# Kernel optimization log

Measured on AMD Instinct MI355X. Metric: run time of the kernel, lower is better.

Reference implementation:

```python
import jax, jax.numpy as jnp
import numpy as np

H = 64; V = 64; INNER = 24; SEQ = 32; CAP = 8
LR = 0.05; BETA1 = 0.9; BETA2 = 0.999; EPS = 1e-8
B = 16384


def setup_inputs():
    key = jax.random.key(0)
    ks = jax.random.split(key, 16)
    def w(k, shape, fan_in):
        return (jax.random.uniform(k, shape, jnp.float32, -1., 1.) / np.sqrt(fan_in)).astype(jnp.float32)
    return {
        "seqs": jax.random.randint(ks[0], (B, SEQ), 0, V),
        "embed": jax.random.normal(ks[1], (V, H), jnp.float32),
        "ff_w1": w(ks[2], (H, 2 * H), H),
        "ff_b1": w(ks[3], (2 * H,), H),
        "ff_w2": w(ks[4], (2 * H, H), 2 * H),
        "ff_b2": w(ks[5], (H,), 2 * H),
        "ln_g": jnp.ones((H,), jnp.float32),
        "ln_b": jnp.zeros((H,), jnp.float32),
        "scorer_w": w(ks[6], (2 * H, 1), 2 * H),
        "scorer_b": w(ks[7], (1,), 2 * H),
        "mlp_w1": w(ks[8], (H, INNER), H),
        "mlp_b1": w(ks[9], (INNER,), H),
        "mlp_w2": w(ks[10], (INNER, H), INNER),
        "mlp_b2": w(ks[11], (H,), INNER),
        "out_w": w(ks[12], (H, V), H),
        "out_b": w(ks[13], (V,), H),
    }


def reference(seqs, embed, ff_w1, ff_b1, ff_w2, ff_b2, ln_g, ln_b,
              scorer_w, scorer_b, mlp_w1, mlp_b1, mlp_w2, mlp_b2, out_w, out_b):
    sg = jax.lax.stop_gradient
    tmap = jax.tree_util.tree_map

    def encode(tok):  # [S] int -> [S,H]
        e = embed[tok]
        f = jnp.maximum(e @ ff_w1 + ff_b1, 0.) @ ff_w2 + ff_b2
        x = e + f
        mu = jnp.mean(x, -1, keepdims=True)
        var = jnp.mean((x - mu) ** 2, -1, keepdims=True)
        return (x - mu) * jax.lax.rsqrt(var + 1e-5) * ln_g + ln_b

    def mlp_fwd(p, x):
        w1, b1, w2, b2 = p
        return jnp.maximum(x @ w1 + b1, 0.) @ w2 + b2

    # tmp MLP is initialized from a detached copy of base mlp params
    base = (sg(mlp_w1), sg(mlp_b1), sg(mlp_w2), sg(mlp_b2))
    ar = jnp.arange(CAP - 1)

    def per_sample(tok):
        h = encode(tok)  # [32,64]
        # pairs: key at even t (0..28), value at odd t (1..29) -> 15 pairs, detached
        keys = sg(h[0:SEQ - 2:2])
        vals = sg(h[1:SEQ - 1:2])
        scores = sg(jnp.concatenate([keys, vals], -1) @ scorer_w[:, 0] + scorer_b[0])  # [15]
        # buffer fills with first CAP pairs, then evict-min (first occurrence) + append
        def evict(carry, new):
            bk, bv, bs = carry
            nk, nv, ns = new
            mi = jnp.argmin(bs)  # first min index, like python min()
            idx = jnp.where(ar < mi, ar, ar + 1)  # pop(mi) shift-left
            return (jnp.concatenate([bk[idx], nk[None]], 0),
                    jnp.concatenate([bv[idx], nv[None]], 0),
                    jnp.concatenate([bs[idx], ns[None]], 0)), None
        (bk, bv, _), _ = jax.lax.scan(
            evict, (keys[:CAP], vals[:CAP], scores[:CAP]),
            (keys[CAP:], vals[CAP:], scores[CAP:]))
        # inner-loop Adam finetune over the CAP buffered (k,v) pairs, in order
        loss = lambda p, k, v: jnp.mean((mlp_fwd(p, k) - v) ** 2)
        def adam(carry, kv):
            p, m, v, t = carry
            g = jax.grad(loss)(p, kv[0], kv[1])
            t = t + 1.
            m = tmap(lambda a, b: BETA1 * a + (1. - BETA1) * b, m, g)
            v = tmap(lambda a, b: BETA2 * a + (1. - BETA2) * b * b, v, g)
            p = tmap(lambda pp, mm, vv: pp - LR * (mm / (1. - BETA1 ** t)) /
                     (jnp.sqrt(vv / (1. - BETA2 ** t)) + EPS), p, m, v)
            return (p, m, v, t), None
        z = tmap(jnp.zeros_like, base)
        (p, _, _, _), _ = jax.lax.scan(adam, (base, z, z, jnp.float32(0.)), (bk, bv))
        # query = encoding of token SEQ-2, through finetuned MLP then output head
        return mlp_fwd(p, h[SEQ - 2]) @ out_w + out_b  # [V]

    return jax.vmap(per_sample)(seqs)  # [B, V]
```

## Files before the change

### kernel.cpp

```cpp
#include <hip/hip_runtime.h>

#define LRC   0.05f
#define B1C   0.9f
#define B2C   0.999f

typedef float v2f __attribute__((ext_vector_type(2)));

__device__ __forceinline__ v2f splat(float s) { v2f r; r.x = s; r.y = s; return r; }

__device__ __forceinline__ float rlane(float v, int l) {
  return __int_as_float(__builtin_amdgcn_readlane(__float_as_int(v), l));
}

template <int CTRL, int RMASK, bool BC>
__device__ __forceinline__ float dpp_add(float x) {
  int y = __builtin_amdgcn_update_dpp(0, __float_as_int(x), CTRL, RMASK, 0xF, BC);
  return x + __int_as_float(y);
}

__device__ __forceinline__ float xrow_sum1(float x) {
#if __has_builtin(__builtin_amdgcn_permlane16_swap)
  {
    unsigned xi = __float_as_uint(x);
    auto a = __builtin_amdgcn_permlane16_swap(xi, xi, false, false);
    x = __uint_as_float(a[0]) + __uint_as_float(a[1]);
  }
#else
  x = x + __int_as_float(__builtin_amdgcn_ds_swizzle(__float_as_int(x), 0x401F));
#endif
#if __has_builtin(__builtin_amdgcn_permlane32_swap)
  {
    unsigned xi = __float_as_uint(x);
    auto b = __builtin_amdgcn_permlane32_swap(xi, xi, false, false);
    x = __uint_as_float(b[0]) + __uint_as_float(b[1]);
  }
#else
  {
    int a32 = ((((int)threadIdx.x & 63) << 2) + 128) & 255;
    x = x + __int_as_float(__builtin_amdgcn_ds_bpermute(a32, __float_as_int(x)));
  }
#endif
  return x;
}

template <int N>
__device__ __forceinline__ void row_sum_batch(float* a) {
  #pragma unroll
  for (int c = 0; c < N; ++c) a[c] = dpp_add<0x121, 0xF, true>(a[c]);
  #pragma unroll
  for (int c = 0; c < N; ++c) a[c] = dpp_add<0x122, 0xF, true>(a[c]);
  #pragma unroll
  for (int c = 0; c < N; ++c) a[c] = dpp_add<0x124, 0xF, true>(a[c]);
  #pragma unroll
  for (int c = 0; c < N; ++c) a[c] = dpp_add<0x128, 0xF, true>(a[c]);
}

__device__ __forceinline__ float wave_sum_repl(float x) {
  x = dpp_add<0x111, 0xF, true>(x);
  x = dpp_add<0x112, 0xF, true>(x);
  x = dpp_add<0x114, 0xF, true>(x);
  x = dpp_add<0x118, 0xF, true>(x);
  x = dpp_add<0x142, 0xa, false>(x);
  x = dpp_add<0x143, 0xc, false>(x);
  return rlane(x, 63);
}

__global__ void enc_kernel(
    const float* __restrict__ embed,
    const float* __restrict__ ff_w1, const float* __restrict__ ff_b1,
    const float* __restrict__ ff_w2, const float* __restrict__ ff_b2,
    const float* __restrict__ ln_g, const float* __restrict__ ln_b,
    const float* __restrict__ scorer_w,
    float* __restrict__ enc, float* __restrict__ sAt, float* __restrict__ sBt)
{
  const int b = blockIdx.x;
  const int lane = threadIdx.x;

  float e = embed[b * 64 + lane];
  float acc0 = ff_b1[lane], acc1 = ff_b1[64 + lane];
  #pragma unroll
  for (int j = 0; j < 64; ++j) {
    float ej = rlane(e, j);
    acc0 = fmaf(ej, ff_w1[j * 128 + lane], acc0);
    acc1 = fmaf(ej, ff_w1[j * 128 + 64 + lane], acc1);
  }
  acc0 = fmaxf(acc0, 0.f);
  acc1 = fmaxf(acc1, 0.f);

  float f = ff_b2[lane];
  #pragma unroll
  for (int l = 0; l < 64; ++l) {
    f = fmaf(rlane(acc0, l), ff_w2[l * 64 + lane], f);
    f = fmaf(rlane(acc1, l), ff_w2[(l + 64) * 64 + lane], f);
  }

  float x = e + f;
  float mu = wave_sum_repl(x) * (1.f / 64.f);
  float d = x - mu;
  float var = wave_sum_repl(d * d) * (1.f / 64.f);
  float h = d * (1.f / sqrtf(var + 1e-5f)) * ln_g[lane] + ln_b[lane];
  enc[b * 64 + lane] = h;

  float sa = wave_sum_repl(h * scorer_w[lane]);
  float sb = wave_sum_repl(h * scorer_w[64 + lane]);
  if (lane == 0) { sAt[b] = sa; sBt[b] = sb; }
}

__device__ __forceinline__ void adam2(v2f& p, v2f& M, v2f& V, v2f g, float lre) {
  M = __builtin_elementwise_fma(M, splat(B1C), g);
  V = __builtin_elementwise_fma(V, splat(B2C), g * g);
  v2f r; r.x = __builtin_amdgcn_rsqf(V.x);
         r.y = __builtin_amdgcn_rsqf(V.y);
  p = __builtin_elementwise_fma(M * r, splat(-lre), p);
}

__global__ __launch_bounds__(256) __attribute__((amdgpu_waves_per_eu(2, 2)))
void adam_kernel(
    const int* __restrict__ seqs, const float* __restrict__ enc,
    const float* __restrict__ sAt, const float* __restrict__ sBt,
    const float* __restrict__ mlp_w1, const float* __restrict__ mlp_b1,
    const float* __restrict__ mlp_w2, const float* __restrict__ mlp_b2,
    const float* __restrict__ out_w, const float* __restrict__ out_b,
    float* __restrict__ out)
{
  const int wid  = threadIdx.x >> 6;
  const int lane = threadIdx.x & 63;
  const int fl = lane & 15, ug = lane >> 4;
  const int c0 = 6 * ug, jb = 4 * fl;
  const int sample = blockIdx.x * 4 + wid;

  constexpr float LRE[8] = {0.05f, 0.0372068f, 0.0319407f, 0.0290564f,
                            0.0272746f, 0.0261060f, 0.0253188f, 0.0247876f};
  constexpr float VINIT = 1e-27f;

  int tv = seqs[sample * 32 + (lane & 31)];

  unsigned skey[15]; int ta[15], tb[15];
  #pragma unroll
  for (int p = 0; p < 15; ++p) {
    ta[p] = __builtin_amdgcn_readlane(tv, 2 * p);
    tb[p] = __builtin_amdgcn_readlane(tv, 2 * p + 1);
    float sf = sAt[ta[p]] + sBt[tb[p]];
    int si = __builtin_amdgcn_readfirstlane(__float_as_int(sf));
    unsigned u = (unsigned)si;
    skey[p] = u ^ (((unsigned)(si >> 31)) | 0x80000000u);
  }
  int q30 = __builtin_amdgcn_readlane(tv, 30);

  unsigned bs[8]; int bka[8], bva[8];
  #pragma unroll
  for (int i = 0; i < 8; ++i) { bs[i] = skey[i]; bka[i] = ta[i]; bva[i] = tb[i]; }
  #pragma unroll
  for (int n = 0; n < 7; ++n) {
    int mi = 0; unsigned ms = bs[0];
    #pragma unroll
    for (int i = 1; i < 8; ++i) {
      if (bs[i] < ms) { mi = i; ms = bs[i]; }
    }
    #pragma unroll
    for (int i = 0; i < 7; ++i) {
      bool sh = i >= mi;
      bs[i]  = sh ? bs[i + 1]  : bs[i];
      bka[i] = sh ? bka[i + 1] : bka[i];
      bva[i] = sh ? bva[i + 1] : bva[i];
    }
    bs[7] = skey[8 + n]; bka[7] = ta[8 + n]; bva[7] = tb[8 + n];
  }

  const float flm = (fl == 0) ? 1.f : 0.f;
  const float ugm = (ug == 0) ? 1.f : 0.f;
  const float S = 2.f / 64.f;

  v2f w1p[4][3], mw1[4][3], vw1[4][3];
  #pragma unroll
  for (int m = 0; m < 4; ++m) {
    const v2f* src = (const v2f*)(mlp_w1 + (jb + m) * 24 + c0);
    #pragma unroll
    for (int p = 0; p < 3; ++p) {
      w1p[m][p] = src[p]; mw1[m][p] = splat(0.f); vw1[m][p] = splat(VINIT);
    }
  }
  v2f w2p[6][2], mw2[6][2], vw2[6][2];
  #pragma unroll
  for (int cc = 0; cc < 6; ++cc) {
    const v2f* src = (const v2f*)(mlp_w2 + (c0 + cc) * 64 + jb);
    #pragma unroll
    for (int p = 0; p < 2; ++p) {
      w2p[cc][p] = src[p]; mw2[cc][p] = splat(0.f); vw2[cc][p] = splat(VINIT);
    }
  }
  v2f b1p[3], mb1[3], vb1[3];
  {
    const v2f* src = (const v2f*)(mlp_b1 + c0);
    #pragma unroll
    for (int p = 0; p < 3; ++p) {
      b1p[p] = src[p] * splat(flm); mb1[p] = splat(0.f); vb1[p] = splat(VINIT);
    }
  }
  v2f b2p[2], mb2[2], vb2[2];
  {
    const v2f* src = (const v2f*)(mlp_b2 + jb);
    #pragma unroll
    for (int p = 0; p < 2; ++p) {
      b2p[p] = src[p] * splat(ugm); mb2[p] = splat(0.f); vb2[p] = splat(VINIT);
    }
  }

  float4 kf = *(const float4*)(enc + bka[0] * 64 + jb);
  float4 vf = *(const float4*)(enc + bva[0] * 64 + jb);
  v2f vn[2];
  vn[0].x = vf.x * -S; vn[0].y = vf.y * -S;
  vn[1].x = vf.z * -S; vn[1].y = vf.w * -S;

  #pragma unroll
  for (int step = 0; step < 8; ++step) {
    const int nidx = (step < 7) ? step + 1 : 7;
    float4 kfn = *(const float4*)(enc + bka[nidx] * 64 + jb);
    float4 vfn = *(const float4*)(enc + bva[nidx] * 64 + jb);

    const float lre = LRE[step];
    const float km[4] = {kf.x, kf.y, kf.z, kf.w};

    v2f t2[3] = {b1p[0], b1p[1], b1p[2]};
    #pragma unroll
    for (int m = 0; m < 4; ++m) {
      v2f km2 = splat(km[m]);
      #pragma unroll
      for (int p = 0; p < 3; ++p) t2[p] = __builtin_elementwise_fma(km2, w1p[m][p], t2[p]);
    }
    float t[6] = {t2[0].x, t2[0].y, t2[1].x, t2[1].y, t2[2].x, t2[2].y};
    row_sum_batch<6>(t);
    float asw[6];
    #pragma unroll
    for (int cc = 0; cc < 6; ++cc) asw[cc] = fmaxf(t[cc], 0.f);

    v2f po2[2];
    #pragma unroll
    for (int p = 0; p < 2; ++p) {
      v2f e0 = b2p[p], e1 = splat(asw[3]) * w2p[3][p];
      e0 = __builtin_elementwise_fma(splat(asw[0]), w2p[0][p], e0);
      e1 = __builtin_elementwise_fma(splat(asw[4]), w2p[4][p], e1);
      e0 = __builtin_elementwise_fma(splat(asw[1]), w2p[1][p], e0);
      e1 = __builtin_elementwise_fma(splat(asw[5]), w2p[5][p], e1);
      e0 = __builtin_elementwise_fma(splat(asw[2]), w2p[2][p], e0);
      po2[p] = e0 + e1;
    }
    #pragma unroll
    for (int p = 0; p < 2; ++p) {
      po2[p].x = xrow_sum1(po2[p].x);
      po2[p].y = xrow_sum1(po2[p].y);
    }
    v2f dout2[2];
    #pragma unroll
    for (int p = 0; p < 2; ++p)
      dout2[p] = __builtin_elementwise_fma(po2[p], splat(S), vn[p]);

    float dh[6];
    #pragma unroll
    for (int cc = 0; cc < 6; ++cc) {
      v2f q = w2p[cc][0] * dout2[0];
      q = __builtin_elementwise_fma(w2p[cc][1], dout2[1], q);
      dh[cc] = q.x + q.y;
    }
    row_sum_batch<6>(dh);
    float dpre[6];
    #pragma unroll
    for (int cc = 0; cc < 6; ++cc)
      dpre[cc] = (asw[cc] > 0.f) ? dh[cc] : 0.f;
    v2f dpre2[3]; dpre2[0].x = dpre[0]; dpre2[0].y = dpre[1];
                  dpre2[1].x = dpre[2]; dpre2[1].y = dpre[3];
                  dpre2[2].x = dpre[4]; dpre2[2].y = dpre[5];

    #pragma unroll
    for (int m = 0; m < 4; ++m) {
      v2f km2 = splat(km[m]);
      #pragma unroll
      for (int p = 0; p < 3; ++p)
        adam2(w1p[m][p], mw1[m][p], vw1[m][p], km2 * dpre2[p], lre);
    }
    #pragma unroll
    for (int cc = 0; cc < 6; ++cc) {
      v2f a2 = splat(asw[cc]);
      #pragma unroll
      for (int p = 0; p < 2; ++p)
        adam2(w2p[cc][p], mw2[cc][p], vw2[cc][p], a2 * dout2[p], lre);
    }
    #pragma unroll
    for (int p = 0; p < 3; ++p)
      adam2(b1p[p], mb1[p], vb1[p], dpre2[p] * splat(flm), lre);
    #pragma unroll
    for (int p = 0; p < 2; ++p)
      adam2(b2p[p], mb2[p], vb2[p], dout2[p] * splat(ugm), lre);

    kf = kfn;
    vn[0].x = vfn.x * -S; vn[0].y = vfn.y * -S;
    vn[1].x = vfn.z * -S; vn[1].y = vfn.w * -S;
  }

  float4 qf = *(const float4*)(enc + q30 * 64 + jb);
  const float qm[4] = {qf.x, qf.y, qf.z, qf.w};
  v2f t2[3] = {b1p[0], b1p[1], b1p[2]};
  #pragma unroll
  for (int m = 0; m < 4; ++m) {
    v2f km2 = splat(qm[m]);
    #pragma unroll
    for (int p = 0; p < 3; ++p) t2[p] = __builtin_elementwise_fma(km2, w1p[m][p], t2[p]);
  }
  float t[6] = {t2[0].x, t2[0].y, t2[1].x, t2[1].y, t2[2].x, t2[2].y};
  row_sum_batch<6>(t);
  float asw[6];
  #pragma unroll
  for (int cc = 0; cc < 6; ++cc) asw[cc] = fmaxf(t[cc], 0.f);
  v2f po2[2];
  #pragma unroll
  for (int p = 0; p < 2; ++p) {
    v2f e0 = b2p[p], e1 = splat(asw[3]) * w2p[3][p];
    e0 = __builtin_elementwise_fma(splat(asw[0]), w2p[0][p], e0);
    e1 = __builtin_elementwise_fma(splat(asw[4]), w2p[4][p], e1);
    e0 = __builtin_elementwise_fma(splat(asw[1]), w2p[1][p], e0);
    e1 = __builtin_elementwise_fma(splat(asw[5]), w2p[5][p], e1);
    e0 = __builtin_elementwise_fma(splat(asw[2]), w2p[2][p], e0);
    po2[p] = e0 + e1;
  }
  #pragma unroll
  for (int p = 0; p < 2; ++p) {
    po2[p].x = xrow_sum1(po2[p].x);
    po2[p].y = xrow_sum1(po2[p].y);
  }
  float po[4] = {po2[0].x, po2[0].y, po2[1].x, po2[1].y};

  float ac0 = out_b[lane], ac1 = 0.f, ac2 = 0.f, ac3 = 0.f;
  #pragma unroll
  for (int l = 0; l < 64; l += 4) {
    ac0 = fmaf(rlane(po[0], l >> 2), out_w[(l    ) * 64 + lane], ac0);
    ac1 = fmaf(rlane(po[1], l >> 2), out_w[(l + 1) * 64 + lane], ac1);
    ac2 = fmaf(rlane(po[2], l >> 2), out_w[(l + 2) * 64 + lane], ac2);
    ac3 = fmaf(rlane(po[3], l >> 2), out_w[(l + 3) * 64 + lane], ac3);
  }
  out[(size_t)sample * 64 + lane] = (ac0 + ac1) + (ac2 + ac3);
}

extern "C" void kernel_launch(void* const* d_in, const int* in_sizes, int n_in,
                              void* d_out, int out_size, void* d_ws, size_t ws_size,
                              hipStream_t stream) {
  const int*   seqs     = (const int*)d_in[0];
  const float* embed    = (const float*)d_in[1];
  const float* ff_w1    = (const float*)d_in[2];
  const float* ff_b1    = (const float*)d_in[3];
  const float* ff_w2    = (const float*)d_in[4];
  const float* ff_b2    = (const float*)d_in[5];
  const float* ln_g     = (const float*)d_in[6];
  const float* ln_b     = (const float*)d_in[7];
  const float* scorer_w = (const float*)d_in[8];
  const float* mlp_w1   = (const float*)d_in[10];
  const float* mlp_b1   = (const float*)d_in[11];
  const float* mlp_w2   = (const float*)d_in[12];
  const float* mlp_b2   = (const float*)d_in[13];
  const float* out_w    = (const float*)d_in[14];
  const float* out_b    = (const float*)d_in[15];

  const int B = in_sizes[0] / 32;
  float* enc = (float*)d_ws;
  float* sAt = enc + 64 * 64;
  float* sBt = sAt + 64;

  enc_kernel<<<64, 64, 0, stream>>>(embed, ff_w1, ff_b1, ff_w2, ff_b2,
                                    ln_g, ln_b, scorer_w, enc, sAt, sBt);
  adam_kernel<<<B / 4, 256, 0, stream>>>(seqs, enc, sAt, sBt,
                                         mlp_w1, mlp_b1, mlp_w2, mlp_b2,
                                         out_w, out_b, (float*)d_out);
}
```

Measured before the change: 211.8 us.

## Split each sample across two waves with LDS cross-wave reduction

Each sample's tiny inner MLP Adam finetune now runs on a 128-thread block (two waves) instead of one wave. Each lane holds half as many parameters (2 H-rows instead of 4), and the hidden-output reduction combines the waves through double-buffered shared memory with a __syncthreads per step. This cuts per-lane register pressure and per-wave serial work and increases the number of waves in flight. The cost is a block barrier each step, duplicated sort and selection work in both waves, and twice as many waves doing the scalar preamble.

Result: slower. 252.8 us (+19.4%).

```diff
diff --git a/kernel.cpp b/kernel.cpp
--- a/kernel.cpp
+++ b/kernel.cpp
@@ -1,6 +1,5 @@
 #include <hip/hip_runtime.h>
 
-#define LRC   0.05f
 #define B1C   0.9f
 #define B2C   0.999f
 
@@ -18,33 +17,29 @@
   return x + __int_as_float(y);
 }
 
-__device__ __forceinline__ float xrow_sum1(float x) {
+__device__ __forceinline__ float addx16(float x) {
 #if __has_builtin(__builtin_amdgcn_permlane16_swap)
-  {
-    unsigned xi = __float_as_uint(x);
-    auto a = __builtin_amdgcn_permlane16_swap(xi, xi, false, false);
-    x = __uint_as_float(a[0]) + __uint_as_float(a[1]);
-  }
+  unsigned xi = __float_as_uint(x);
+  auto a = __builtin_amdgcn_permlane16_swap(xi, xi, false, false);
+  return __uint_as_float(a[0]) + __uint_as_float(a[1]);
 #else
-  x = x + __int_as_float(__builtin_amdgcn_ds_swizzle(__float_as_int(x), 0x401F));
+  return x + __int_as_float(__builtin_amdgcn_ds_swizzle(__float_as_int(x), 0x401F));
 #endif
+}
+
+__device__ __forceinline__ float addx32(float x) {
 #if __has_builtin(__builtin_amdgcn_permlane32_swap)
-  {
-    unsigned xi = __float_as_uint(x);
-    auto b = __builtin_amdgcn_permlane32_swap(xi, xi, false, false);
-    x = __uint_as_float(b[0]) + __uint_as_float(b[1]);
-  }
+  unsigned xi = __float_as_uint(x);
+  auto b = __builtin_amdgcn_permlane32_swap(xi, xi, false, false);
+  return __uint_as_float(b[0]) + __uint_as_float(b[1]);
 #else
-  {
-    int a32 = ((((int)threadIdx.x & 63) << 2) + 128) & 255;
-    x = x + __int_as_float(__builtin_amdgcn_ds_bpermute(a32, __float_as_int(x)));
-  }
+  int a32 = ((((int)threadIdx.x & 63) ^ 32) << 2);
+  return x + __int_as_float(__builtin_amdgcn_ds_bpermute(a32, __float_as_int(x)));
 #endif
-  return x;
 }
 
 template <int N>
-__device__ __forceinline__ void row_sum_batch(float* a) {
+__device__ __forceinline__ void row_sum32_batch(float* a) {
   #pragma unroll
   for (int c = 0; c < N; ++c) a[c] = dpp_add<0x121, 0xF, true>(a[c]);
   #pragma unroll
@@ -53,6 +48,8 @@
   for (int c = 0; c < N; ++c) a[c] = dpp_add<0x124, 0xF, true>(a[c]);
   #pragma unroll
   for (int c = 0; c < N; ++c) a[c] = dpp_add<0x128, 0xF, true>(a[c]);
+  #pragma unroll
+  for (int c = 0; c < N; ++c) a[c] = addx16(a[c]);
 }
 
 __device__ __forceinline__ float wave_sum_repl(float x) {
@@ -114,8 +111,7 @@
   p = __builtin_elementwise_fma(M * r, splat(-lre), p);
 }
 
-__global__ __launch_bounds__(256) __attribute__((amdgpu_waves_per_eu(2, 2)))
-void adam_kernel(
+__global__ __launch_bounds__(128, 3) void adam_kernel(
     const int* __restrict__ seqs, const float* __restrict__ enc,
     const float* __restrict__ sAt, const float* __restrict__ sBt,
     const float* __restrict__ mlp_w1, const float* __restrict__ mlp_b1,
@@ -123,17 +119,23 @@
     const float* __restrict__ out_w, const float* __restrict__ out_b,
     float* __restrict__ out)
 {
-  const int wid  = threadIdx.x >> 6;
-  const int lane = threadIdx.x & 63;
-  const int fl = lane & 15, ug = lane >> 4;
-  const int c0 = 6 * ug, jb = 4 * fl;
-  const int sample = blockIdx.x * 4 + wid;
+  const int tid  = threadIdx.x;
+  const int wave = tid >> 6;
+  const int lane = tid & 63;
+  const int flg  = lane & 31;
+  const int ugw  = lane >> 5;
+  const int ug   = wave * 2 + ugw;
+  const int c0   = 6 * ug;
+  const int jb   = 2 * flg;
+  const int sample = blockIdx.x;
+
+  __shared__ v2f pobuf[2][128];
 
   constexpr float LRE[8] = {0.05f, 0.0372068f, 0.0319407f, 0.0290564f,
                             0.0272746f, 0.0261060f, 0.0253188f, 0.0247876f};
   constexpr float VINIT = 1e-27f;
 
-  int tv = seqs[sample * 32 + (lane & 31)];
+  int tv = seqs[sample * 32 + flg];
 
   unsigned skey[15]; int ta[15], tb[15];
   #pragma unroll
@@ -167,27 +169,24 @@
     bs[7] = skey[8 + n]; bka[7] = ta[8 + n]; bva[7] = tb[8 + n];
   }
 
-  const float flm = (fl == 0) ? 1.f : 0.f;
-  const float ugm = (ug == 0) ? 1.f : 0.f;
+  const float flm = (flg == 0) ? 1.f : 0.f;
+  const float ugm = (ug  == 0) ? 1.f : 0.f;
   const float S = 2.f / 64.f;
 
-  v2f w1p[4][3], mw1[4][3], vw1[4][3];
-  #pragma unroll
-  for (int m = 0; m < 4; ++m) {
+  v2f w1p[2][3], mw1[2][3], vw1[2][3];
+  #pragma unroll
+  for (int m = 0; m < 2; ++m) {
     const v2f* src = (const v2f*)(mlp_w1 + (jb + m) * 24 + c0);
     #pragma unroll
     for (int p = 0; p < 3; ++p) {
       w1p[m][p] = src[p]; mw1[m][p] = splat(0.f); vw1[m][p] = splat(VINIT);
     }
   }
-  v2f w2p[6][2], mw2[6][2], vw2[6][2];
+  v2f w2p[6], mw2[6], vw2[6];
   #pragma unroll
   for (int cc = 0; cc < 6; ++cc) {
-    const v2f* src = (const v2f*)(mlp_w2 + (c0 + cc) * 64 + jb);
-    #pragma unroll
-    for (int p = 0; p < 2; ++p) {
-      w2p[cc][p] = src[p]; mw2[cc][p] = splat(0.f); vw2[cc][p] = splat(VINIT);
-    }
+    w2p[cc] = *(const v2f*)(mlp_w2 + (c0 + cc) * 64 + jb);
+    mw2[cc] = splat(0.f); vw2[cc] = splat(VINIT);
   }
   v2f b1p[3], mb1[3], vb1[3];
   {
@@ -197,72 +196,59 @@
       b1p[p] = src[p] * splat(flm); mb1[p] = splat(0.f); vb1[p] = splat(VINIT);
     }
   }
-  v2f b2p[2], mb2[2], vb2[2];
-  {
-    const v2f* src = (const v2f*)(mlp_b2 + jb);
-    #pragma unroll
-    for (int p = 0; p < 2; ++p) {
-      b2p[p] = src[p] * splat(ugm); mb2[p] = splat(0.f); vb2[p] = splat(VINIT);
-    }
-  }
-
-  float4 kf = *(const float4*)(enc + bka[0] * 64 + jb);
-  float4 vf = *(const float4*)(enc + bva[0] * 64 + jb);
-  v2f vn[2];
-  vn[0].x = vf.x * -S; vn[0].y = vf.y * -S;
-  vn[1].x = vf.z * -S; vn[1].y = vf.w * -S;
+  v2f b2p, mb2, vb2;
+  b2p = (*(const v2f*)(mlp_b2 + jb)) * splat(ugm);
+  mb2 = splat(0.f); vb2 = splat(VINIT);
+
+  float2 kf = *(const float2*)(enc + bka[0] * 64 + jb);
+  float2 vf = *(const float2*)(enc + bva[0] * 64 + jb);
+  v2f vn; vn.x = vf.x * -S; vn.y = vf.y * -S;
 
   #pragma unroll
   for (int step = 0; step < 8; ++step) {
     const int nidx = (step < 7) ? step + 1 : 7;
-    float4 kfn = *(const float4*)(enc + bka[nidx] * 64 + jb);
-    float4 vfn = *(const float4*)(enc + bva[nidx] * 64 + jb);
+    float2 kfn = *(const float2*)(enc + bka[nidx] * 64 + jb);
+    float2 vfn = *(const float2*)(enc + bva[nidx] * 64 + jb);
 
     const float lre = LRE[step];
-    const float km[4] = {kf.x, kf.y, kf.z, kf.w};
+    const float km[2] = {kf.x, kf.y};
 
     v2f t2[3] = {b1p[0], b1p[1], b1p[2]};
     #pragma unroll
-    for (int m = 0; m < 4; ++m) {
+    for (int m = 0; m < 2; ++m) {
       v2f km2 = splat(km[m]);
       #pragma unroll
       for (int p = 0; p < 3; ++p) t2[p] = __builtin_elementwise_fma(km2, w1p[m][p], t2[p]);
     }
     float t[6] = {t2[0].x, t2[0].y, t2[1].x, t2[1].y, t2[2].x, t2[2].y};
-    row_sum_batch<6>(t);
+    row_sum32_batch<6>(t);
     float asw[6];
     #pragma unroll
     for (int cc = 0; cc < 6; ++cc) asw[cc] = fmaxf(t[cc], 0.f);
 
-    v2f po2[2];
-    #pragma unroll
-    for (int p = 0; p < 2; ++p) {
-      v2f e0 = b2p[p], e1 = splat(asw[3]) * w2p[3][p];
-      e0 = __builtin_elementwise_fma(splat(asw[0]), w2p[0][p], e0);
-      e1 = __builtin_elementwise_fma(splat(asw[4]), w2p[4][p], e1);
-      e0 = __builtin_elementwise_fma(splat(asw[1]), w2p[1][p], e0);
-      e1 = __builtin_elementwise_fma(splat(asw[5]), w2p[5][p], e1);
-      e0 = __builtin_elementwise_fma(splat(asw[2]), w2p[2][p], e0);
-      po2[p] = e0 + e1;
-    }
-    #pragma unroll
-    for (int p = 0; p < 2; ++p) {
-      po2[p].x = xrow_sum1(po2[p].x);
-      po2[p].y = xrow_sum1(po2[p].y);
-    }
-    v2f dout2[2];
-    #pragma unroll
-    for (int p = 0; p < 2; ++p)
-      dout2[p] = __builtin_elementwise_fma(po2[p], splat(S), vn[p]);
+    v2f e0 = b2p, e1 = splat(asw[3]) * w2p[3];
+    e0 = __builtin_elementwise_fma(splat(asw[0]), w2p[0], e0);
+    e1 = __builtin_elementwise_fma(splat(asw[4]), w2p[4], e1);
+    e0 = __builtin_elementwise_fma(splat(asw[1]), w2p[1], e0);
+    e1 = __builtin_elementwise_fma(splat(asw[5]), w2p[5], e1);
+    e0 = __builtin_elementwise_fma(splat(asw[2]), w2p[2], e0);
+    v2f po = e0 + e1;
+
+    po.x = addx32(po.x);
+    po.y = addx32(po.y);
+    pobuf[step & 1][tid] = po;
+    __syncthreads();
+    po += pobuf[step & 1][tid ^ 64];
+
+    v2f dout = __builtin_elementwise_fma(po, splat(S), vn);
 
     float dh[6];
     #pragma unroll
     for (int cc = 0; cc < 6; ++cc) {
-      v2f q = w2p[cc][0] * dout2[0];
-      q = __builtin_elementwise_fma(w2p[cc][1], dout2[1], q);
+      v2f q = w2p[cc] * dout;
       dh[cc] = q.x + q.y;
     }
-    row_sum_batch<6>(dh);
+    row_sum32_batch<6>(dh);
     float dpre[6];
     #pragma unroll
     for (int cc = 0; cc < 6; ++cc)
@@ -272,72 +258,62 @@
                   dpre2[2].x = dpre[4]; dpre2[2].y = dpre[5];
 
     #pragma unroll
-    for (int m = 0; m < 4; ++m) {
+    for (int m = 0; m < 2; ++m) {
       v2f km2 = splat(km[m]);
       #pragma unroll
       for (int p = 0; p < 3; ++p)
         adam2(w1p[m][p], mw1[m][p], vw1[m][p], km2 * dpre2[p], lre);
     }
     #pragma unroll
-    for (int cc = 0; cc < 6; ++cc) {
-      v2f a2 = splat(asw[cc]);
-      #pragma unroll
-      for (int p = 0; p < 2; ++p)
-        adam2(w2p[cc][p], mw2[cc][p], vw2[cc][p], a2 * dout2[p], lre);
-    }
+    for (int cc = 0; cc < 6; ++cc)
+      adam2(w2p[cc], mw2[cc], vw2[cc], splat(asw[cc]) * dout, lre);
     #pragma unroll
     for (int p = 0; p < 3; ++p)
       adam2(b1p[p], mb1[p], vb1[p], dpre2[p] * splat(flm), lre);
-    #pragma unroll
-    for (int p = 0; p < 2; ++p)
-      adam2(b2p[p], mb2[p], vb2[p], dout2[p] * splat(ugm), lre);
+    adam2(b2p, mb2, vb2, dout * splat(ugm), lre);
 
     kf = kfn;
-    vn[0].x = vfn.x * -S; vn[0].y = vfn.y * -S;
-    vn[1].x = vfn.z * -S; vn[1].y = vfn.w * -S;
-  }
-
-  float4 qf = *(const float4*)(enc + q30 * 64 + jb);
-  const float qm[4] = {qf.x, qf.y, qf.z, qf.w};
+    vn.x = vfn.x * -S; vn.y = vfn.y * -S;
+  }
+
+  float2 qf = *(const float2*)(enc + q30 * 64 + jb);
+  const float qm[2] = {qf.x, qf.y};
   v2f t2[3] = {b1p[0], b1p[1], b1p[2]};
   #pragma unroll
-  for (int m = 0; m < 4; ++m) {
+  for (int m = 0; m < 2; ++m) {
     v2f km2 = splat(qm[m]);
     #pragma unroll
     for (int p = 0; p < 3; ++p) t2[p] = __builtin_elementwise_fma(km2, w1p[m][p], t2[p]);
   }
   float t[6] = {t2[0].x, t2[0].y, t2[1].x, t2[1].y, t2[2].x, t2[2].y};
-  row_sum_batch<6>(t);
+  row_sum32_batch<6>(t);
   float asw[6];
   #pragma unroll
   for (int cc = 0; cc < 6; ++cc) asw[cc] = fmaxf(t[cc], 0.f);
-  v2f po2[2];
-  #pragma unroll
-  for (int p = 0; p < 2; ++p) {
-    v2f e0 = b2p[p], e1 = splat(asw[3]) * w2p[3][p];
-    e0 = __builtin_elementwise_fma(splat(asw[0]), w2p[0][p], e0);
-    e1 = __builtin_elementwise_fma(splat(asw[4]), w2p[4][p], e1);
-    e0 = __builtin_elementwise_fma(splat(asw[1]), w2p[1][p], e0);
-    e1 = __builtin_elementwise_fma(splat(asw[5]), w2p[5][p], e1);
-    e0 = __builtin_elementwise_fma(splat(asw[2]), w2p[2][p], e0);
-    po2[p] = e0 + e1;
-  }
-  #pragma unroll
-  for (int p = 0; p < 2; ++p) {
-    po2[p].x = xrow_sum1(po2[p].x);
-    po2[p].y = xrow_sum1(po2[p].y);
-  }
-  float po[4] = {po2[0].x, po2[0].y, po2[1].x, po2[1].y};
-
-  float ac0 = out_b[lane], ac1 = 0.f, ac2 = 0.f, ac3 = 0.f;
-  #pragma unroll
-  for (int l = 0; l < 64; l += 4) {
-    ac0 = fmaf(rlane(po[0], l >> 2), out_w[(l    ) * 64 + lane], ac0);
-    ac1 = fmaf(rlane(po[1], l >> 2), out_w[(l + 1) * 64 + lane], ac1);
-    ac2 = fmaf(rlane(po[2], l >> 2), out_w[(l + 2) * 64 + lane], ac2);
-    ac3 = fmaf(rlane(po[3], l >> 2), out_w[(l + 3) * 64 + lane], ac3);
-  }
-  out[(size_t)sample * 64 + lane] = (ac0 + ac1) + (ac2 + ac3);
+  v2f e0 = b2p, e1 = splat(asw[3]) * w2p[3];
+  e0 = __builtin_elementwise_fma(splat(asw[0]), w2p[0], e0);
+  e1 = __builtin_elementwise_fma(splat(asw[4]), w2p[4], e1);
+  e0 = __builtin_elementwise_fma(splat(asw[1]), w2p[1], e0);
+  e1 = __builtin_elementwise_fma(splat(asw[5]), w2p[5], e1);
+  e0 = __builtin_elementwise_fma(splat(asw[2]), w2p[2], e0);
+  v2f po = e0 + e1;
+  po.x = addx32(po.x);
+  po.y = addx32(po.y);
+  pobuf[0][tid] = po;
+  __syncthreads();
+  po += pobuf[0][tid ^ 64];
+
+  if (wave == 0) {
+    float ac0 = out_b[lane], ac1 = 0.f, ac2 = 0.f, ac3 = 0.f;
+    #pragma unroll
+    for (int q = 0; q < 32; q += 2) {
+      ac0 = fmaf(rlane(po.x, q),     out_w[(2 * q    ) * 64 + lane], ac0);
+      ac1 = fmaf(rlane(po.y, q),     out_w[(2 * q + 1) * 64 + lane], ac1);
+      ac2 = fmaf(rlane(po.x, q + 1), out_w[(2 * q + 2) * 64 + lane], ac2);
+      ac3 = fmaf(rlane(po.y, q + 1), out_w[(2 * q + 3) * 64 + lane], ac3);
+    }
+    out[(size_t)sample * 64 + lane] = (ac0 + ac1) + (ac2 + ac3);
+  }
 }
 
 extern "C" void kernel_launch(void* const* d_in, const int* in_sizes, int n_in,
@@ -366,7 +342,7 @@
 
   enc_kernel<<<64, 64, 0, stream>>>(embed, ff_w1, ff_b1, ff_w2, ff_b2,
                                     ln_g, ln_b, scorer_w, enc, sAt, sBt);
-  adam_kernel<<<B / 4, 256, 0, stream>>>(seqs, enc, sAt, sBt,
-                                         mlp_w1, mlp_b1, mlp_w2, mlp_b2,
-                                         out_w, out_b, (float*)d_out);
-}
+  adam_kernel<<<B, 128, 0, stream>>>(seqs, enc, sAt, sBt,
+                                     mlp_w1, mlp_b1, mlp_w2, mlp_b2,
+                                     out_w, out_b, (float*)d_out);
+}
```
